# Kernel tuning notes

Hardware: AMD Instinct MI355X
Metric: run time of the kernel (lower is better)

## Reference

```python
import jax, jax.numpy as jnp
import numpy as np

B, N, M, C, H = 131072, 6, 3, 2, 64
DT, ALPHA, BETA, KAPPA = 0.01, 0.5, 2.0, 0.0
NOISE_EPS = 1e-7


def setup_inputs() -> dict:
    key = jax.random.key(0)
    ks = jax.random.split(key, 7)
    x = jax.random.normal(ks[0], (B, N), dtype=jnp.float32)
    A = 0.1 * jax.random.normal(ks[1], (B, N, N), dtype=jnp.float32)
    # PD covariance so the (single) Cholesky succeeds, matching the torch happy path
    P = jnp.einsum('bij,bkj->bik', A, A) + 0.1 * jnp.eye(N, dtype=jnp.float32)
    u = jax.random.normal(ks[2], (B, C), dtype=jnp.float32)
    y = jax.random.normal(ks[3], (B, M), dtype=jnp.float32)
    LQ = 0.1 * jnp.eye(N, dtype=jnp.float32)
    LR = 0.1 * jnp.eye(M, dtype=jnp.float32)
    W1 = 0.1 * jax.random.normal(ks[4], (N + C, H), dtype=jnp.float32)
    b1 = jnp.zeros((H,), jnp.float32)
    W2 = 0.1 * jax.random.normal(ks[5], (H, N), dtype=jnp.float32)
    b2 = jnp.zeros((N,), jnp.float32)
    return dict(x=x, P=P, u=u, y=y, LQ=LQ, LR=LR, W1=W1, b1=b1, W2=W2, b2=b2)


def _dynamics(x, u, W1, b1, W2, b2):
    # learned vehicle dynamics: MLP over [state, control]
    h = jnp.tanh(jnp.concatenate([x, u], axis=-1) @ W1 + b1)
    return h @ W2 + b2


def _rk4_step(x, u, dt, params):
    k1 = _dynamics(x, u, *params)
    k2 = _dynamics(x + dt / 2.0 * k1, u, *params)
    k3 = _dynamics(x + dt / 2.0 * k2, u, *params)
    k4 = _dynamics(x + dt * k3, u, *params)
    return x + dt / 6.0 * (k1 + 2 * k2 + 2 * k3 + k4)


def _ukf_forward(x, P, u, y, LQ, LR, W1, b1, W2, b2):
    n, m = N, M
    lam = ALPHA ** 2 * (n + KAPPA) - n
    I_n = jnp.eye(n, dtype=x.dtype)
    I_m = jnp.eye(m, dtype=x.dtype)

    # --- sigma points (vectorized over all 2n+1 points) ---
    P_sym = 0.5 * (P + jnp.swapaxes(P, -1, -2))
    base = (n + lam) * P_sym + 1e-5 * I_n
    sqrt_P = jnp.linalg.cholesky(base)                       # (B, n, n)
    cols = jnp.swapaxes(sqrt_P, -1, -2)                      # (B, n, n), cols[:, i] = i-th column
    sigma = jnp.concatenate(
        [x[:, None, :], x[:, None, :] + cols, x[:, None, :] - cols], axis=1
    )                                                         # (B, 2n+1, n)
    S_pts = 2 * n + 1
    w = 1.0 / (2.0 * (n + lam))
    Wm = jnp.full((S_pts,), w, dtype=x.dtype).at[0].set(lam / (n + lam))
    Wc = jnp.full((S_pts,), w, dtype=x.dtype).at[0].set(lam / (n + lam) + (1 - ALPHA ** 2 + BETA))

    # --- propagate all sigma points through RK4 at once ---
    params = (W1, b1, W2, b2)
    u_b = jnp.broadcast_to(u[:, None, :], (x.shape[0], S_pts, C))
    sigma_pred = _rk4_step(sigma, u_b, DT, params)            # (B, 2n+1, n)

    x_pred = jnp.einsum('s,bsi->bi', Wm, sigma_pred)
    dx = sigma_pred - x_pred[:, None, :]
    LQt = jnp.tril(LQ)
    Q = LQt @ LQt.T + NOISE_EPS * I_n
    P_pred = jnp.einsum('s,bsi,bsj->bij', Wc, dx, dx) + Q

    # --- measurement: first m states ---
    sigma_meas = sigma_pred[..., :m]                          # (B, 2n+1, m)
    y_pred = jnp.einsum('s,bsi->bi', Wm, sigma_meas)
    dy = sigma_meas - y_pred[:, None, :]
    LRt = jnp.tril(LR)
    R = LRt @ LRt.T + NOISE_EPS * I_m
    S = jnp.einsum('s,bsi,bsj->bij', Wc, dy, dy) + R
    cross = jnp.einsum('s,bsi,bsj->bij', Wc, dx, dy)

    S_inv = jnp.linalg.inv(S + 1e-5 * I_m)
    K = cross @ S_inv                                         # (B, n, m)
    innov = y - y_pred
    x_updated = x_pred + jnp.einsum('bij,bj->bi', K, innov)
    P_updated = P_pred - K @ S @ jnp.swapaxes(K, -1, -2)
    P_updated = 0.5 * (P_updated + jnp.swapaxes(P_updated, -1, -2)) + 1e-4 * I_n
    return x_updated, P_updated, x_pred, P_pred, y_pred, S, K


def reference(x, P, u, y, LQ, LR, W1, b1, W2, b2):
    return _ukf_forward(x, P, u, y, LQ, LR, W1, b1, W2, b2)
```

## Files before the change

kernel.cpp:

```cpp
#include <hip/hip_runtime.h>
#include <math.h>

typedef __attribute__((ext_vector_type(8)))  short bf16x8;
typedef __attribute__((ext_vector_type(4)))  float f32x4;
typedef __attribute__((ext_vector_type(16))) float f32x16;
typedef __attribute__((ext_vector_type(2)))  float f32x2;

#define TRI(i,j) (((i)*((i)+1))/2 + (j))
#define ONE3 0.3333333333333333f
#define QOFF 6144
#define LOFF 8192

static __device__ __forceinline__ unsigned short f2b(float f) {
  union { float f; unsigned u; } v; v.f = f;
  unsigned r = v.u + 0x7FFFu + ((v.u >> 16) & 1u);
  return (unsigned short)(r >> 16);
}
static __device__ __forceinline__ unsigned pk2(float lo, float hi) {
  return (unsigned)f2b(lo) | ((unsigned)f2b(hi) << 16);
}
static __device__ __forceinline__ unsigned pk2t(float lo, float hi) {
  return __builtin_amdgcn_perm(__float_as_uint(hi), __float_as_uint(lo), 0x07060302u);
}

#define TC0 0.970866f
#define TC1 (-0.217815f)
#define TC2 0.028904f
#define TC3 (-0.0014079f)

static __device__ __forceinline__ unsigned tanh2_pk(float a, float b) {
#if __has_builtin(__builtin_elementwise_fma)
  f32x2 z; z[0] = a; z[1] = b;
  f32x2 k3 = {TC3, TC3}, k2 = {TC2, TC2}, k1 = {TC1, TC1}, k0 = {TC0, TC0};
  f32x2 t = z * z;
  f32x2 p = __builtin_elementwise_fma(t, k3, k2);
  p = __builtin_elementwise_fma(p, t, k1);
  p = __builtin_elementwise_fma(p, t, k0);
  f32x2 r = z * p;
  return pk2t(r[0], r[1]);
#else
  float ta = a * a, tb = b * b;
  float pa = fmaf(fmaf(fmaf(TC3, ta, TC2), ta, TC1), ta, TC0);
  float pb = fmaf(fmaf(fmaf(TC3, tb, TC2), tb, TC1), tb, TC0);
  return pk2t(a * pa, b * pb);
#endif
}

__global__ void pack_frags(const float* __restrict__ W1, const float* __restrict__ b1,
                           const float* __restrict__ W2,
                           const float* __restrict__ LQ, const float* __restrict__ LR,
                           char* __restrict__ ws) {
  int lane = threadIdx.x;
  int mr = lane & 31, u = lane >> 5;
  unsigned* A1 = (unsigned*)(ws + lane * 96);
  unsigned* A2 = (unsigned*)(ws + lane * 96 + 32);
#pragma unroll
  for (int t = 0; t < 2; ++t) {
    int h = 32 * t + mr;
    if (u == 0) {
#pragma unroll
      for (int p = 0; p < 4; ++p)
        A1[t * 4 + p] = pk2(W1[(2 * p) * 64 + h], W1[(2 * p + 1) * 64 + h]);
    } else {
      A1[t * 4 + 0] = pk2(b1[h], 0.0f);
      A1[t * 4 + 1] = 0u; A1[t * 4 + 2] = 0u; A1[t * 4 + 3] = 0u;
    }
  }
#pragma unroll
  for (int kq = 0; kq < 4; ++kq) {
#pragma unroll
    for (int p = 0; p < 4; ++p) {
      float lo = (mr < 6) ? W2[(16 * kq + 8 * u + 2 * p) * 6 + mr] : 0.0f;
      float hi = (mr < 6) ? W2[(16 * kq + 8 * u + 2 * p + 1) * 6 + mr] : 0.0f;
      A2[kq * 4 + p] = pk2(lo, hi);
    }
  }
  if (lane == 0) {
    float* qo = (float*)(ws + QOFF);
    for (int i = 0; i < 6; ++i)
      for (int j = 0; j <= i; ++j) {
        float s = (i == j) ? 1e-7f : 0.0f;
        for (int k = 0; k <= j; ++k) s = fmaf(LQ[i * 6 + k], LQ[j * 6 + k], s);
        qo[TRI(i, j)] = s;
      }
    for (int i = 0; i < 3; ++i)
      for (int j = 0; j <= i; ++j) {
        float s = (i == j) ? 1e-7f : 0.0f;
        for (int k = 0; k <= j; ++k) s = fmaf(LR[i * 3 + k], LR[j * 3 + k], s);
        qo[21 + TRI(i, j)] = s;
      }
  }
}

__global__ void prep_chol(const float* __restrict__ gP, float* __restrict__ Lbuf, int B) {
  int b = blockIdx.x * blockDim.x + threadIdx.x;
  if (b >= B) return;
  float Pf[36];
  const float4* p4 = (const float4*)(gP + (size_t)b * 36);
#pragma unroll
  for (int q = 0; q < 9; ++q) {
    float4 v = p4[q];
    Pf[q*4+0]=v.x; Pf[q*4+1]=v.y; Pf[q*4+2]=v.z; Pf[q*4+3]=v.w;
  }
  float base[21], Lt[21];
#pragma unroll
  for (int i = 0; i < 6; ++i)
#pragma unroll
    for (int j = 0; j <= i; ++j)
      base[TRI(i,j)] = 0.75f * (Pf[i*6+j] + Pf[j*6+i]) + ((i==j) ? 1e-5f : 0.0f);
#pragma unroll
  for (int k = 0; k < 6; ++k) {
    float s = base[TRI(k,k)];
#pragma unroll
    for (int m2 = 0; m2 < k; ++m2) s = fmaf(-Lt[TRI(k,m2)], Lt[TRI(k,m2)], s);
    float d = sqrtf(s);
    Lt[TRI(k,k)] = d;
    float inv = 1.0f / d;
#pragma unroll
    for (int i = k + 1; i < 6; ++i) {
      float s2 = base[TRI(i,k)];
#pragma unroll
      for (int m2 = 0; m2 < k; ++m2) s2 = fmaf(-Lt[TRI(i,m2)], Lt[TRI(k,m2)], s2);
      Lt[TRI(i,k)] = s2 * inv;
    }
  }
  float* lp = Lbuf + (size_t)b * 40;
#pragma unroll
  for (int c = 0; c < 6; ++c)
#pragma unroll
    for (int f = 0; f < 6; ++f)
      lp[c * 6 + f] = (f >= c) ? Lt[TRI(f, c)] : 0.0f;
}

__launch_bounds__(256, 4)
__global__ void ukf_main(const float* __restrict__ gx,
                         const float* __restrict__ gu,
                         const float* __restrict__ gb2,
                         const float* __restrict__ Lbuf,
                         const char*  __restrict__ ws,
                         float* __restrict__ Ubuf, int B) {
  __shared__ f32x4 ldsv[4][136];
  int lane = threadIdx.x & 63;
  int wid  = threadIdx.x >> 6;
  int p    = blockIdx.x * 4 + wid;
  if (2 * p >= B) return;
  int u   = lane >> 5;
  int c   = lane & 31;
  int q16 = lane >> 4, m16 = lane & 15;
  int bc  = 2 * p + ((lane >> 4) & 1);
  float* dxs = (float*)&ldsv[wid][0];

  int   sidx = c & 15;
  float sgn = (sidx == 0 || sidx > 12) ? 0.0f : ((sidx <= 6) ? 1.0f : -1.0f);
  int   cc  = (sidx >= 1 && sidx <= 6) ? (sidx - 1) : ((sidx >= 7) ? (sidx - 7) : 0);
  const float* lp = Lbuf + (size_t)bc * 40 + cc * 6;
  float Lc[6];
#pragma unroll
  for (int f = 0; f < 6; ++f) Lc[f] = lp[f];

  float x0c[6];
  {
    const float* xb = gx + (size_t)bc * 6;
    float2 t0 = *(const float2*)(xb);
    float2 t1 = *(const float2*)(xb + 2);
    float2 t2 = *(const float2*)(xb + 4);
    x0c[0]=t0.x; x0c[1]=t0.y; x0c[2]=t1.x; x0c[3]=t1.y; x0c[4]=t2.x; x0c[5]=t2.y;
  }
  float2 uu = *(const float2*)(gu + (size_t)bc * 2);
  unsigned uu_pk = pk2(uu.x, uu.y);

  const char* wp = ws + lane * 96;
  bf16x8 A1v0 = *((const bf16x8*)wp);
  bf16x8 A1v1 = *((const bf16x8*)(wp + 16));
  bf16x8 A2v[4];
#pragma unroll
  for (int kq = 0; kq < 4; ++kq) A2v[kq] = *((const bf16x8*)(wp + 32 + kq * 16));
  float b2r[6];
#pragma unroll
  for (int i = 0; i < 6; ++i) b2r[i] = gb2[i];

  float sgnL[6], xs[6];
#pragma unroll
  for (int f = 0; f < 6; ++f) { sgnL[f] = sgn * Lc[f]; xs[f] = x0c[f] + sgnL[f]; }

  float kf[6]   = {0,0,0,0,0,0};
  float ksum[6] = {0,0,0,0,0,0};
  f32x16 z16;
#pragma unroll
  for (int i = 0; i < 16; ++i) z16[i] = 0.0f;
#pragma unroll
  for (int st = 0; st < 4; ++st) {
    const float cin = (st == 3) ? 0.01f : 0.005f;
    float xi[6];
#pragma unroll
    for (int f = 0; f < 6; ++f) xi[f] = fmaf(cin, kf[f], xs[f]);
    union { bf16x8 v; unsigned w[4]; } bx;
    bx.w[0] = u ? 0x00003F80u : pk2t(xi[0], xi[1]);
    bx.w[1] = pk2t(xi[2], xi[3]);
    bx.w[2] = pk2t(xi[4], xi[5]);
    bx.w[3] = uu_pk;
    f32x16 d1a = __builtin_amdgcn_mfma_f32_32x32x16_bf16(A1v0, bx.v, z16, 0, 0, 0);
    f32x16 d1b = __builtin_amdgcn_mfma_f32_32x32x16_bf16(A1v1, bx.v, z16, 0, 0, 0);
    unsigned Hpk[16];
#pragma unroll
    for (int pr = 0; pr < 8; ++pr) Hpk[pr]     = tanh2_pk(d1a[2*pr], d1a[2*pr+1]);
#pragma unroll
    for (int pr = 0; pr < 8; ++pr) Hpk[8 + pr] = tanh2_pk(d1b[2*pr], d1b[2*pr+1]);
    f32x16 d2 = z16;
#pragma unroll
    for (int kq = 0; kq < 4; ++kq) {
      int base = 8 * (kq >> 1) + 4 * (kq & 1);
      unsigned vA = u ? Hpk[base + 0] : Hpk[base + 2];
      unsigned vB = u ? Hpk[base + 1] : Hpk[base + 3];
      unsigned rA = __shfl_xor(vA, 32, 64);
      unsigned rB = __shfl_xor(vB, 32, 64);
      union { bf16x8 v; unsigned w[4]; } bh;
      bh.w[0] = u ? rA : Hpk[base + 0];
      bh.w[1] = u ? rB : Hpk[base + 1];
      bh.w[2] = u ? Hpk[base + 2] : rA;
      bh.w[3] = u ? Hpk[base + 3] : rB;
      d2 = __builtin_amdgcn_mfma_f32_32x32x16_bf16(A2v[kq], bh.v, d2, 0, 0, 0);
    }
    float e0 = __shfl_xor(d2[0], 32, 64);
    float e1 = __shfl_xor(d2[1], 32, 64);
    float e2 = __shfl_xor(d2[2], 32, 64);
    float e3 = __shfl_xor(d2[3], 32, 64);
    kf[0] = (u ? e0 : d2[0]) + b2r[0];
    kf[1] = (u ? e1 : d2[1]) + b2r[1];
    kf[2] = (u ? e2 : d2[2]) + b2r[2];
    kf[3] = (u ? e3 : d2[3]) + b2r[3];
    kf[4] = (u ? d2[0] : e0) + b2r[4];
    kf[5] = (u ? d2[1] : e1) + b2r[5];
    const float wks = (st == 0 || st == 3) ? 1.0f : 2.0f;
#pragma unroll
    for (int f = 0; f < 6; ++f) ksum[f] = fmaf(wks, kf[f], ksum[f]);
  }

  const float dt6 = 0.01f / 6.0f;
  if (u == 0) {
#pragma unroll
    for (int f = 0; f < 6; ++f) dxs[c * 17 + f] = fmaf(dt6, ksum[f], sgnL[f]);
  }

  float dxv[8];
#pragma unroll
  for (int j = 0; j < 8; ++j) dxv[j] = dxs[(8 * q16 + j) * 17 + m16];
  float wc0[8], wc1[8];
#pragma unroll
  for (int j = 0; j < 8; ++j) {
    float c0j = (j == 0) ? -0.25f : ONE3;
    float c1j = (j <= 4) ? ONE3 : 0.0f;
    wc0[j] = (q16 == 0) ? c0j : ((q16 == 1) ? c1j : 0.0f);
    wc1[j] = (q16 == 2) ? c0j : ((q16 == 3) ? c1j : 0.0f);
  }
  float wm00 = (q16 == 0) ? -3.0f : wc0[0];
  float wm10 = (q16 == 2) ? -3.0f : wc1[0];
  bool mlt6 = (m16 < 6), m6 = (m16 == 6), m7 = (m16 == 7);
  union { bf16x8 v; unsigned w[4]; } am0, am1, bw;
  {
    float a0[8], a1[8];
#pragma unroll
    for (int j = 0; j < 8; ++j) {
      float wmj0 = (j == 0) ? wm00 : wc0[j];
      float wmj1 = (j == 0) ? wm10 : wc1[j];
      float alt0 = m6 ? wc0[j] : (m7 ? wmj0 : 0.0f);
      float alt1 = m6 ? wc1[j] : (m7 ? wmj1 : 0.0f);
      a0[j] = mlt6 ? wc0[j] * dxv[j] : alt0;
      a1[j] = mlt6 ? wc1[j] * dxv[j] : alt1;
    }
#pragma unroll
    for (int pr = 0; pr < 4; ++pr) {
      am0.w[pr] = pk2(a0[2*pr], a0[2*pr+1]);
      am1.w[pr] = pk2(a1[2*pr], a1[2*pr+1]);
      bw.w[pr]  = pk2(dxv[2*pr], dxv[2*pr+1]);
    }
  }
  f32x4 zz = {0.0f, 0.0f, 0.0f, 0.0f};
  f32x4 Dm0 = __builtin_amdgcn_mfma_f32_16x16x32_bf16(am0.v, bw.v, zz, 0, 0, 0);
  f32x4 Dm1 = __builtin_amdgcn_mfma_f32_16x16x32_bf16(am1.v, bw.v, zz, 0, 0, 0);

  if (q16 < 2 && m16 < 6) {
    float* u0 = Ubuf + (size_t)(2 * p) * 48;
    float* u1 = Ubuf + (size_t)(2 * p + 1) * 48;
#pragma unroll
    for (int i = 0; i < 4; ++i) {
      u0[(4 * q16 + i) * 6 + m16] = Dm0[i];
      u1[(4 * q16 + i) * 6 + m16] = Dm1[i];
    }
  }
}

__global__ void ukf_epi(const float* __restrict__ gx,
                        const float* __restrict__ gy,
                        const char*  __restrict__ ws,
                        const float* __restrict__ Ubuf,
                        float* __restrict__ out, int B) {
  int b = blockIdx.x * blockDim.x + threadIdx.x;
  if (b >= B) return;
  const float* rec = Ubuf + (size_t)b * 48;
  float U[21], cbv[6], dbv[6];
#pragma unroll
  for (int i = 0; i < 6; ++i)
#pragma unroll
    for (int j = 0; j <= i; ++j) U[TRI(i,j)] = rec[i * 6 + j];
#pragma unroll
  for (int j = 0; j < 6; ++j) { cbv[j] = rec[36 + j]; dbv[j] = rec[42 + j]; }

  float x0[6];
  {
    const float* xb = gx + (size_t)b * 6;
    float2 t0 = *(const float2*)(xb);
    float2 t1 = *(const float2*)(xb + 2);
    float2 t2 = *(const float2*)(xb + 4);
    x0[0]=t0.x; x0[1]=t0.y; x0[2]=t1.x; x0[3]=t1.y; x0[4]=t2.x; x0[5]=t2.y;
  }
  const float* yb = gy + (size_t)b * 3;
  float yy0 = yb[0], yy1 = yb[1], yy2 = yb[2];

  const float* qro = (const float*)(ws + QOFF);
  float Qm[21], Rm[6];
#pragma unroll
  for (int t = 0; t < 21; ++t) Qm[t] = qro[t];
#pragma unroll
  for (int t = 0; t < 6; ++t) Rm[t] = qro[21 + t];

  float xp[6];
#pragma unroll
  for (int i = 0; i < 6; ++i) xp[i] = x0[i] + dbv[i];
  float D[21];
#pragma unroll
  for (int i = 0; i < 6; ++i)
#pragma unroll
    for (int j = 0; j <= i; ++j) {
      float v = U[TRI(i,j)];
      v -= cbv[i] * dbv[j];
      v -= dbv[i] * cbv[j];
      v = fmaf(3.75f * dbv[i], dbv[j], v);
      D[TRI(i,j)] = v;
    }
  float s00 = D[TRI(0,0)] + Rm[TRI(0,0)];
  float s10 = D[TRI(1,0)] + Rm[TRI(1,0)];
  float s11 = D[TRI(1,1)] + Rm[TRI(1,1)];
  float s20 = D[TRI(2,0)] + Rm[TRI(2,0)];
  float s21 = D[TRI(2,1)] + Rm[TRI(2,1)];
  float s22 = D[TRI(2,2)] + Rm[TRI(2,2)];
  float a00 = s00 + 1e-5f, a11 = s11 + 1e-5f, a22 = s22 + 1e-5f;
  float a10 = s10, a20 = s20, a21 = s21;
  float adj00 = a11*a22 - a21*a21;
  float adj01 = a20*a21 - a10*a22;
  float adj02 = a10*a21 - a11*a20;
  float adj11 = a00*a22 - a20*a20;
  float adj12 = a10*a20 - a00*a21;
  float adj22 = a00*a11 - a10*a10;
  float det  = a00*adj00 + a10*adj01 + a20*adj02;
  float idet = 1.0f / det;
  float I00 = adj00*idet, I01 = adj01*idet, I02 = adj02*idet;
  float I11 = adj11*idet, I12 = adj12*idet, I22 = adj22*idet;

#define DS(i,j) ((i) >= (j) ? D[TRI(i,j)] : D[TRI(j,i)])
  float K_[18];
#pragma unroll
  for (int i = 0; i < 6; ++i) {
    float c0 = DS(i,0), c1 = DS(i,1), c2 = DS(i,2);
    K_[i*3+0] = c0*I00 + c1*I01 + c2*I02;
    K_[i*3+1] = c0*I01 + c1*I11 + c2*I12;
    K_[i*3+2] = c0*I02 + c1*I12 + c2*I22;
  }
  float inn0 = yy0 - xp[0], inn1 = yy1 - xp[1], inn2 = yy2 - xp[2];
  float xu[6];
#pragma unroll
  for (int i = 0; i < 6; ++i)
    xu[i] = xp[i] + K_[i*3]*inn0 + K_[i*3+1]*inn1 + K_[i*3+2]*inn2;

  float KS[18];
#pragma unroll
  for (int i = 0; i < 6; ++i) {
    float k0 = K_[i*3], k1 = K_[i*3+1], k2 = K_[i*3+2];
    KS[i*3+0] = k0*s00 + k1*s10 + k2*s20;
    KS[i*3+1] = k0*s10 + k1*s11 + k2*s21;
    KS[i*3+2] = k0*s20 + k1*s21 + k2*s22;
  }
  float Pu[21];
#pragma unroll
  for (int i = 0; i < 6; ++i)
#pragma unroll
    for (int j = 0; j <= i; ++j) {
      float v = D[TRI(i,j)] + Qm[TRI(i,j)];
      v -= KS[i*3]*K_[j*3] + KS[i*3+1]*K_[j*3+1] + KS[i*3+2]*K_[j*3+2];
      Pu[TRI(i,j)] = v + ((i==j) ? 1e-4f : 0.0f);
    }

  float* o_xu = out;
  float* o_Pu = out + (size_t)6  * B;
  float* o_xp = out + (size_t)42 * B;
  float* o_Pp = out + (size_t)48 * B;
  float* o_yp = out + (size_t)84 * B;
  float* o_S  = out + (size_t)87 * B;
  float* o_K  = out + (size_t)96 * B;
  {
    float* pp = o_xu + (size_t)b * 6;
    ((float2*)pp)[0] = make_float2(xu[0], xu[1]);
    ((float2*)pp)[1] = make_float2(xu[2], xu[3]);
    ((float2*)pp)[2] = make_float2(xu[4], xu[5]);
  }
  {
    float* pp = o_Pu + (size_t)b * 36;
#pragma unroll
    for (int i = 0; i < 6; ++i)
#pragma unroll
      for (int j = 0; j < 6; j += 2) {
        float v0 = (i>=j)   ? Pu[TRI(i,j)]   : Pu[TRI(j,i)];
        float v1 = (i>=j+1) ? Pu[TRI(i,j+1)] : Pu[TRI(j+1,i)];
        *(float2*)(pp + i*6 + j) = make_float2(v0, v1);
      }
  }
  {
    float* pp = o_xp + (size_t)b * 6;
    ((float2*)pp)[0] = make_float2(xp[0], xp[1]);
    ((float2*)pp)[1] = make_float2(xp[2], xp[3]);
    ((float2*)pp)[2] = make_float2(xp[4], xp[5]);
  }
  {
    float* pp = o_Pp + (size_t)b * 36;
#pragma unroll
    for (int i = 0; i < 6; ++i)
#pragma unroll
      for (int j = 0; j < 6; j += 2) {
        float v0 = ((i>=j)   ? D[TRI(i,j)]   : D[TRI(j,i)])   + ((i>=j)   ? Qm[TRI(i,j)]   : Qm[TRI(j,i)]);
        float v1 = ((i>=j+1) ? D[TRI(i,j+1)] : D[TRI(j+1,i)]) + ((i>=j+1) ? Qm[TRI(i,j+1)] : Qm[TRI(j+1,i)]);
        *(float2*)(pp + i*6 + j) = make_float2(v0, v1);
      }
  }
  {
    float* pp = o_yp + (size_t)b * 3;
    pp[0] = xp[0]; pp[1] = xp[1]; pp[2] = xp[2];
  }
  {
    float* pp = o_S + (size_t)b * 9;
    pp[0]=s00; pp[1]=s10; pp[2]=s20;
    pp[3]=s10; pp[4]=s11; pp[5]=s21;
    pp[6]=s20; pp[7]=s21; pp[8]=s22;
  }
  {
    float* pp = o_K + (size_t)b * 18;
#pragma unroll
    for (int i = 0; i < 9; ++i)
      ((float2*)pp)[i] = make_float2(K_[i*2], K_[i*2+1]);
  }
}

extern "C" void kernel_launch(void* const* d_in, const int* in_sizes, int n_in,
                              void* d_out, int out_size, void* d_ws, size_t ws_size,
                              hipStream_t stream) {
  const float* x  = (const float*)d_in[0];
  const float* P  = (const float*)d_in[1];
  const float* u  = (const float*)d_in[2];
  const float* y  = (const float*)d_in[3];
  const float* LQ = (const float*)d_in[4];
  const float* LR = (const float*)d_in[5];
  const float* W1 = (const float*)d_in[6];
  const float* b1 = (const float*)d_in[7];
  const float* W2 = (const float*)d_in[8];
  const float* b2 = (const float*)d_in[9];
  float* out = (float*)d_out;
  char*  ws  = (char*)d_ws;
  int B = in_sizes[0] / 6;

  float* Lbuf = (float*)(ws + LOFF);
  float* Ubuf = (float*)(ws + LOFF + (size_t)B * 160);

  hipLaunchKernelGGL(pack_frags, dim3(1), dim3(64), 0, stream, W1, b1, W2, LQ, LR, ws);
  hipLaunchKernelGGL(prep_chol, dim3((B + 255) / 256), dim3(256), 0, stream, P, Lbuf, B);
  hipLaunchKernelGGL(ukf_main, dim3((B + 7) / 8), dim3(256), 0, stream,
                     x, u, b2, (const float*)Lbuf, (const char*)ws, Ubuf, B);
  hipLaunchKernelGGL(ukf_epi, dim3((B + 255) / 256), dim3(256), 0, stream,
                     x, y, (const char*)ws, (const float*)Ubuf, out, B);
}
```

Baseline: 240.7 us.

## Fuse fragment packing into Cholesky prep and drop shuffles in RK4 MLP

Merges the single-block weight-packing kernel into the Cholesky prep kernel, removing one launch. The W2 fragment layout is reordered so the tanh hidden outputs feed the second MFMA directly, which removes the cross-half lane shuffles for each k-block. The b2 bias is folded into the stage base states and the final offset, and the k-sum is accumulated in MFMA output layout, so the output shuffles are skipped on the last RK4 stage. The cost is more involved index bookkeeping in the packed layout.

Result: faster. 234.3 us (-2.6%).

```diff
diff --git a/kernel.cpp b/kernel.cpp
--- a/kernel.cpp
+++ b/kernel.cpp
@@ -46,53 +46,56 @@
 #endif
 }
 
-__global__ void pack_frags(const float* __restrict__ W1, const float* __restrict__ b1,
-                           const float* __restrict__ W2,
-                           const float* __restrict__ LQ, const float* __restrict__ LR,
-                           char* __restrict__ ws) {
-  int lane = threadIdx.x;
-  int mr = lane & 31, u = lane >> 5;
-  unsigned* A1 = (unsigned*)(ws + lane * 96);
-  unsigned* A2 = (unsigned*)(ws + lane * 96 + 32);
-#pragma unroll
-  for (int t = 0; t < 2; ++t) {
-    int h = 32 * t + mr;
-    if (u == 0) {
-#pragma unroll
-      for (int p = 0; p < 4; ++p)
-        A1[t * 4 + p] = pk2(W1[(2 * p) * 64 + h], W1[(2 * p + 1) * 64 + h]);
-    } else {
-      A1[t * 4 + 0] = pk2(b1[h], 0.0f);
-      A1[t * 4 + 1] = 0u; A1[t * 4 + 2] = 0u; A1[t * 4 + 3] = 0u;
-    }
-  }
-#pragma unroll
-  for (int kq = 0; kq < 4; ++kq) {
-#pragma unroll
-    for (int p = 0; p < 4; ++p) {
-      float lo = (mr < 6) ? W2[(16 * kq + 8 * u + 2 * p) * 6 + mr] : 0.0f;
-      float hi = (mr < 6) ? W2[(16 * kq + 8 * u + 2 * p + 1) * 6 + mr] : 0.0f;
-      A2[kq * 4 + p] = pk2(lo, hi);
-    }
-  }
-  if (lane == 0) {
-    float* qo = (float*)(ws + QOFF);
-    for (int i = 0; i < 6; ++i)
-      for (int j = 0; j <= i; ++j) {
-        float s = (i == j) ? 1e-7f : 0.0f;
-        for (int k = 0; k <= j; ++k) s = fmaf(LQ[i * 6 + k], LQ[j * 6 + k], s);
-        qo[TRI(i, j)] = s;
+__global__ void prep_kernel(const float* __restrict__ gP,
+                            const float* __restrict__ W1, const float* __restrict__ b1,
+                            const float* __restrict__ W2,
+                            const float* __restrict__ LQ, const float* __restrict__ LR,
+                            char* __restrict__ ws, float* __restrict__ Lbuf, int B) {
+  if (blockIdx.x == 0 && threadIdx.x < 64) {
+    int lane = threadIdx.x;
+    int mr = lane & 31, u = lane >> 5;
+    unsigned* A1 = (unsigned*)(ws + lane * 96);
+    unsigned* A2 = (unsigned*)(ws + lane * 96 + 32);
+#pragma unroll
+    for (int t = 0; t < 2; ++t) {
+      int h = 32 * t + mr;
+      if (u == 0) {
+#pragma unroll
+        for (int p = 0; p < 4; ++p)
+          A1[t * 4 + p] = pk2(W1[(2 * p) * 64 + h], W1[(2 * p + 1) * 64 + h]);
+      } else {
+        A1[t * 4 + 0] = pk2(b1[h], 0.0f);
+        A1[t * 4 + 1] = 0u; A1[t * 4 + 2] = 0u; A1[t * 4 + 3] = 0u;
       }
-    for (int i = 0; i < 3; ++i)
-      for (int j = 0; j <= i; ++j) {
-        float s = (i == j) ? 1e-7f : 0.0f;
-        for (int k = 0; k <= j; ++k) s = fmaf(LR[i * 3 + k], LR[j * 3 + k], s);
-        qo[21 + TRI(i, j)] = s;
+    }
+#pragma unroll
+    for (int kq = 0; kq < 4; ++kq) {
+#pragma unroll
+      for (int p = 0; p < 4; ++p) {
+        int rm = 2 * p + ((p >= 2) ? 4 : 0);
+        int hid = 32 * (kq >> 1) + 16 * (kq & 1) + 4 * u + rm;
+        float lo = (mr < 6) ? W2[hid * 6 + mr] : 0.0f;
+        float hi = (mr < 6) ? W2[(hid + 1) * 6 + mr] : 0.0f;
+        A2[kq * 4 + p] = pk2(lo, hi);
       }
-  }
-}
-
-__global__ void prep_chol(const float* __restrict__ gP, float* __restrict__ Lbuf, int B) {
+    }
+    if (lane == 0) {
+      float* qo = (float*)(ws + QOFF);
+      for (int i = 0; i < 6; ++i)
+        for (int j = 0; j <= i; ++j) {
+          float s = (i == j) ? 1e-7f : 0.0f;
+          for (int k = 0; k <= j; ++k) s = fmaf(LQ[i * 6 + k], LQ[j * 6 + k], s);
+          qo[TRI(i, j)] = s;
+        }
+      for (int i = 0; i < 3; ++i)
+        for (int j = 0; j <= i; ++j) {
+          float s = (i == j) ? 1e-7f : 0.0f;
+          for (int k = 0; k <= j; ++k) s = fmaf(LR[i * 3 + k], LR[j * 3 + k], s);
+          qo[21 + TRI(i, j)] = s;
+        }
+    }
+  }
+
   int b = blockIdx.x * blockDim.x + threadIdx.x;
   if (b >= B) return;
   float Pf[36];
@@ -153,10 +156,11 @@
   int   sidx = c & 15;
   float sgn = (sidx == 0 || sidx > 12) ? 0.0f : ((sidx <= 6) ? 1.0f : -1.0f);
   int   cc  = (sidx >= 1 && sidx <= 6) ? (sidx - 1) : ((sidx >= 7) ? (sidx - 7) : 0);
-  const float* lp = Lbuf + (size_t)bc * 40 + cc * 6;
+  if (cc > 5) cc = 5;
+  const float* lpr = Lbuf + (size_t)bc * 40 + cc * 6;
   float Lc[6];
 #pragma unroll
-  for (int f = 0; f < 6; ++f) Lc[f] = lp[f];
+  for (int f = 0; f < 6; ++f) Lc[f] = lpr[f];
 
   float x0c[6];
   {
@@ -179,26 +183,28 @@
 #pragma unroll
   for (int i = 0; i < 6; ++i) b2r[i] = gb2[i];
 
-  float sgnL[6], xs[6];
-#pragma unroll
-  for (int f = 0; f < 6; ++f) { sgnL[f] = sgn * Lc[f]; xs[f] = x0c[f] + sgnL[f]; }
-
-  float kf[6]   = {0,0,0,0,0,0};
-  float ksum[6] = {0,0,0,0,0,0};
+  float xs[6], sgnLp[6], xs005[6];
+#pragma unroll
+  for (int f = 0; f < 6; ++f) {
+    float sl = sgn * Lc[f];
+    xs[f] = x0c[f] + sl;
+    sgnLp[f] = fmaf(0.01f, b2r[f], sl);
+  }
+  union { bf16x8 v; unsigned w[4]; } bx;
+  bx.w[0] = u ? 0x00003F80u : pk2t(xs[0], xs[1]);
+  bx.w[1] = pk2t(xs[2], xs[3]);
+  bx.w[2] = pk2t(xs[4], xs[5]);
+  bx.w[3] = uu_pk;
+#pragma unroll
+  for (int f = 0; f < 6; ++f) xs005[f] = fmaf(0.005f, b2r[f], xs[f]);
+
   f32x16 z16;
 #pragma unroll
   for (int i = 0; i < 16; ++i) z16[i] = 0.0f;
+
+  float ksum[4] = {0.f, 0.f, 0.f, 0.f};
 #pragma unroll
   for (int st = 0; st < 4; ++st) {
-    const float cin = (st == 3) ? 0.01f : 0.005f;
-    float xi[6];
-#pragma unroll
-    for (int f = 0; f < 6; ++f) xi[f] = fmaf(cin, kf[f], xs[f]);
-    union { bf16x8 v; unsigned w[4]; } bx;
-    bx.w[0] = u ? 0x00003F80u : pk2t(xi[0], xi[1]);
-    bx.w[1] = pk2t(xi[2], xi[3]);
-    bx.w[2] = pk2t(xi[4], xi[5]);
-    bx.w[3] = uu_pk;
     f32x16 d1a = __builtin_amdgcn_mfma_f32_32x32x16_bf16(A1v0, bx.v, z16, 0, 0, 0);
     f32x16 d1b = __builtin_amdgcn_mfma_f32_32x32x16_bf16(A1v1, bx.v, z16, 0, 0, 0);
     unsigned Hpk[16];
@@ -209,37 +215,51 @@
     f32x16 d2 = z16;
 #pragma unroll
     for (int kq = 0; kq < 4; ++kq) {
-      int base = 8 * (kq >> 1) + 4 * (kq & 1);
-      unsigned vA = u ? Hpk[base + 0] : Hpk[base + 2];
-      unsigned vB = u ? Hpk[base + 1] : Hpk[base + 3];
-      unsigned rA = __shfl_xor(vA, 32, 64);
-      unsigned rB = __shfl_xor(vB, 32, 64);
       union { bf16x8 v; unsigned w[4]; } bh;
-      bh.w[0] = u ? rA : Hpk[base + 0];
-      bh.w[1] = u ? rB : Hpk[base + 1];
-      bh.w[2] = u ? Hpk[base + 2] : rA;
-      bh.w[3] = u ? Hpk[base + 3] : rB;
+      bh.w[0] = Hpk[4*kq+0]; bh.w[1] = Hpk[4*kq+1];
+      bh.w[2] = Hpk[4*kq+2]; bh.w[3] = Hpk[4*kq+3];
       d2 = __builtin_amdgcn_mfma_f32_32x32x16_bf16(A2v[kq], bh.v, d2, 0, 0, 0);
     }
-    float e0 = __shfl_xor(d2[0], 32, 64);
-    float e1 = __shfl_xor(d2[1], 32, 64);
-    float e2 = __shfl_xor(d2[2], 32, 64);
-    float e3 = __shfl_xor(d2[3], 32, 64);
-    kf[0] = (u ? e0 : d2[0]) + b2r[0];
-    kf[1] = (u ? e1 : d2[1]) + b2r[1];
-    kf[2] = (u ? e2 : d2[2]) + b2r[2];
-    kf[3] = (u ? e3 : d2[3]) + b2r[3];
-    kf[4] = (u ? d2[0] : e0) + b2r[4];
-    kf[5] = (u ? d2[1] : e1) + b2r[5];
     const float wks = (st == 0 || st == 3) ? 1.0f : 2.0f;
 #pragma unroll
-    for (int f = 0; f < 6; ++f) ksum[f] = fmaf(wks, kf[f], ksum[f]);
+    for (int g = 0; g < 4; ++g) ksum[g] = fmaf(wks, d2[g], ksum[g]);
+    if (st < 3) {
+      float e0 = __shfl_xor(d2[0], 32, 64);
+      float e1 = __shfl_xor(d2[1], 32, 64);
+      float e2 = __shfl_xor(d2[2], 32, 64);
+      float e3 = __shfl_xor(d2[3], 32, 64);
+      float k0 = u ? e0 : d2[0];
+      float k1 = u ? e1 : d2[1];
+      float k2 = u ? e2 : d2[2];
+      float k3 = u ? e3 : d2[3];
+      float k4 = u ? d2[0] : e0;
+      float k5 = u ? d2[1] : e1;
+      const float cin = (st == 2) ? 0.01f : 0.005f;
+      float base0, base1, base2, base3, base4, base5;
+      if (st == 2) {
+        base0 = fmaf(0.005f, b2r[0], xs005[0]); base1 = fmaf(0.005f, b2r[1], xs005[1]);
+        base2 = fmaf(0.005f, b2r[2], xs005[2]); base3 = fmaf(0.005f, b2r[3], xs005[3]);
+        base4 = fmaf(0.005f, b2r[4], xs005[4]); base5 = fmaf(0.005f, b2r[5], xs005[5]);
+      } else {
+        base0 = xs005[0]; base1 = xs005[1]; base2 = xs005[2];
+        base3 = xs005[3]; base4 = xs005[4]; base5 = xs005[5];
+      }
+      float xi0 = fmaf(cin, k0, base0), xi1 = fmaf(cin, k1, base1);
+      float xi2 = fmaf(cin, k2, base2), xi3 = fmaf(cin, k3, base3);
+      float xi4 = fmaf(cin, k4, base4), xi5 = fmaf(cin, k5, base5);
+      bx.w[0] = u ? 0x00003F80u : pk2t(xi0, xi1);
+      bx.w[1] = pk2t(xi2, xi3);
+      bx.w[2] = pk2t(xi4, xi5);
+    }
   }
 
   const float dt6 = 0.01f / 6.0f;
   if (u == 0) {
 #pragma unroll
-    for (int f = 0; f < 6; ++f) dxs[c * 17 + f] = fmaf(dt6, ksum[f], sgnL[f]);
+    for (int g = 0; g < 4; ++g) dxs[c * 17 + g] = fmaf(dt6, ksum[g], sgnLp[g]);
+  } else {
+#pragma unroll
+    for (int g = 0; g < 2; ++g) dxs[c * 17 + 4 + g] = fmaf(dt6, ksum[g], sgnLp[4 + g]);
   }
 
   float dxv[8];
@@ -469,8 +489,8 @@
   float* Lbuf = (float*)(ws + LOFF);
   float* Ubuf = (float*)(ws + LOFF + (size_t)B * 160);
 
-  hipLaunchKernelGGL(pack_frags, dim3(1), dim3(64), 0, stream, W1, b1, W2, LQ, LR, ws);
-  hipLaunchKernelGGL(prep_chol, dim3((B + 255) / 256), dim3(256), 0, stream, P, Lbuf, B);
+  hipLaunchKernelGGL(prep_kernel, dim3((B + 255) / 256), dim3(256), 0, stream,
+                     P, W1, b1, W2, LQ, LR, ws, Lbuf, B);
   hipLaunchKernelGGL(ukf_main, dim3((B + 7) / 8), dim3(256), 0, stream,
                      x, u, b2, (const float*)Lbuf, (const char*)ws, Ubuf, B);
   hipLaunchKernelGGL(ukf_epi, dim3((B + 255) / 256), dim3(256), 0, stream,
```
